# Kernel tuning notes

Measured on AMD Instinct MI355X. Metric: run time of the kernel, lower is better.

Reference implementation:

```python
import jax, jax.numpy as jnp
import numpy as np

N = 100000
N1 = 12500  # N // K clusters after one downsample
K = 8
CHANNELS = [256, 128, 64, 32, 3]


def _conv(f, idx, kern, bias, act):
    # gather K neighbors and flatten: [M, K*Cin]
    g = f[idx].reshape(idx.shape[0], -1)
    out = g @ kern.T + bias
    return jax.nn.sigmoid(out) if act else out


def setup_inputs() -> dict:
    key = jax.random.key(0)
    ks = jax.random.split(key, 16)
    inp = {
        "features": jax.random.normal(ks[0], (N, 256), dtype=jnp.float32),
        "knn_idx0": jax.random.randint(ks[1], (N, K), 0, N, dtype=jnp.int32),
        "knn_idx1": jax.random.randint(ks[2], (N1, K), 0, N1, dtype=jnp.int32),
        "labels": jax.random.randint(ks[3], (N,), 0, N1, dtype=jnp.int32),
    }
    cin = 256
    for i, cout in enumerate(CHANNELS):
        inp[f"k{i}"] = jax.random.normal(ks[4 + i], (cout, K * cin), dtype=jnp.float32) * 0.1
        inp[f"b{i}"] = jnp.zeros((1, cout), dtype=jnp.float32)
        cin = cout
    return inp


def reference(features, knn_idx0, knn_idx1, labels, k0, b0, k1, b1, k2, b2, k3, b3, k4, b4):
    f = features
    # layer 0 (full resolution)
    f = _conv(f, knn_idx0, k0, b0, act=True)
    # layer 1: downsample via scatter-mean over kmeans labels
    s = jax.ops.segment_sum(f, labels, num_segments=N1)
    cnt = jax.ops.segment_sum(jnp.ones((f.shape[0], 1), f.dtype), labels, num_segments=N1)
    f = s / jnp.maximum(cnt, 1.0)
    f = _conv(f, knn_idx1, k1, b1, act=True)
    # layer 2 (coarse resolution)
    f = _conv(f, knn_idx1, k2, b2, act=True)
    # layer 3: upsample by indexing cluster features back to points
    f = f[labels]
    f = _conv(f, knn_idx0, k3, b3, act=True)
    # layer 4: final, no sigmoid
    f = _conv(f, knn_idx0, k4, b4, act=False)
    return f
```

## Files before the change

kernel.cpp:

```cpp
#include <hip/hip_runtime.h>
#include <hip/hip_bf16.h>


typedef __attribute__((ext_vector_type(8))) _Float16 f16x8;
typedef __attribute__((ext_vector_type(4))) float f32x4;
typedef __attribute__((ext_vector_type(8))) unsigned short u16x8;

#define NPTS 100000
#define N1PTS 12500

__device__ __forceinline__ void gload_lds16(const unsigned short* g, unsigned short* l) {
  __builtin_amdgcn_global_load_lds(
      (const __attribute__((address_space(1))) void*)g,
      (__attribute__((address_space(3))) void*)l, 16, 0, 0);
}

__device__ __forceinline__ int swz(int r, int k) {
  return r * 64 + ((((k >> 3) ^ r) & 7) << 3) + (k & 7);
}

__device__ __forceinline__ unsigned short f16bits(float x) {
  return __builtin_bit_cast(unsigned short, (_Float16)x);
}

__global__ void prepack_w(const float* __restrict__ W, unsigned short* __restrict__ out,
                          int n) {
  int i = blockIdx.x * 256 + threadIdx.x;
  if (i < n) out[i] = f16bits(W[i]);
}

__global__ void prepack_w0(const float* __restrict__ W, unsigned short* __restrict__ out) {
  const int tid = blockIdx.x * 256 + threadIdx.x;
  const int l = tid & 63;
  const int s = (tid >> 6) & 1;
  const int n = (tid >> 7) & 3;
  const int w = (tid >> 9) & 3;
  const int c = tid >> 11;
  const int co = w * 64 + n * 16 + (l & 15);
  const int k = c * 64 + s * 32 + ((l >> 4) << 3);
  const float* src = W + (size_t)co * 2048 + k;
  u16x8 h;
#pragma unroll
  for (int e = 0; e < 8; ++e) h[e] = f16bits(src[e]);
  ((u16x8*)out)[tid] = h;
}

__global__ void prepack_feat(const float* __restrict__ F, unsigned short* __restrict__ out,
                             int n8) {
  int i = blockIdx.x * 256 + threadIdx.x;
  if (i >= n8) return;
  const float4* s = (const float4*)(F + (size_t)i * 8);
  float4 v0 = s[0], v1 = s[1];
  float x[8] = {v0.x, v0.y, v0.z, v0.w, v1.x, v1.y, v1.z, v1.w};
  u16x8 o;
#pragma unroll
  for (int e = 0; e < 8; ++e) o[e] = f16bits(x[e]);
  ((u16x8*)out)[i] = o;
}

__global__ void count_labels(const int* __restrict__ labels, int* __restrict__ cnt) {
  int i = blockIdx.x * 256 + threadIdx.x;
  if (i < NPTS) atomicAdd(&cnt[labels[i]], 1);
}

__global__ void compose_idx(const int* __restrict__ knn0, const int* __restrict__ labels,
                            int* __restrict__ out) {
  int i = blockIdx.x * 256 + threadIdx.x;
  if (i < NPTS * 8) out[i] = labels[knn0[i]];
}

__global__ void finalize_pool(const int* __restrict__ pool, const int* __restrict__ cnt,
                              unsigned short* __restrict__ out) {
  int i = blockIdx.x * 256 + threadIdx.x;
  if (i >= N1PTS * 256) return;
  float denom = fmaxf((float)cnt[i >> 8], 1.0f);
  out[i] = f16bits(((float)pool[i]) * (1.0f / 16777216.0f) / denom);
}

__global__ void finalize_splitk(const int* __restrict__ acc, const float* __restrict__ bias,
                                unsigned short* __restrict__ out, int n, int cmask) {
  int i = blockIdx.x * 256 + threadIdx.x;
  if (i >= n) return;
  float z = ((float)acc[i]) * (1.0f / 4194304.0f) + bias[i & cmask];
  out[i] = f16bits(1.0f / (1.0f + expf(-z)));
}

__global__ __launch_bounds__(256, 3) void conv0_gemm(
    const unsigned short* __restrict__ F16, const int* __restrict__ idx,
    const int* __restrict__ lab, const unsigned short* __restrict__ Wpk,
    const float* __restrict__ bias, int* __restrict__ pool) {
  __shared__ alignas(16) unsigned short sA[4][64 * 64];

  const int t = threadIdx.x;
  const int w = t >> 6, l = t & 63;
  const int lr = l & 15, lh = l >> 4;
  const int row0 = blockIdx.x * 64;

  const int srow8 = l >> 3;
  const int sseg_src = (l & 7) ^ (srow8 & 7);

  const unsigned ldsbase = (unsigned)(uintptr_t)&sA[0][0];
  unsigned aoff[4][2];
#pragma unroll
  for (int m = 0; m < 4; ++m)
#pragma unroll
    for (int s = 0; s < 2; ++s)
      aoff[m][s] =
          ldsbase + (((m * 16 + lr) * 64 + ((((s << 2) + lh) ^ (lr & 7)) << 3)) << 1);

  const f16x8* wp8 = (const f16x8*)Wpk + (size_t)w * 512 + l;

  auto ldnb = [&](int cc, int q) -> int {
    int grow = row0 + w * 16 + q * 8 + srow8;
    grow = grow < NPTS ? grow : NPTS - 1;
    return idx[grow * 8 + ((cc & 31) >> 2)];
  };
  auto stage_q = [&](int cc, int nb, int q) {
    const unsigned short* gp =
        F16 + ((size_t)nb << 8) + ((cc & 3) << 6) + sseg_src * 8;
    unsigned short* lp = &sA[cc & 3][(w * 16 + q * 8) * 64];
    gload_lds16(gp, lp);
  };

  f32x4 acc[4][4] = {};
  f16x8 bh[2][4];

  int n00 = ldnb(0, 0), n01 = ldnb(0, 1);
  int n10 = ldnb(1, 0), n11 = ldnb(1, 1);
  int nc0 = ldnb(2, 0), nc1 = ldnb(2, 1);
  __builtin_amdgcn_sched_barrier(0);
#pragma unroll
  for (int s = 0; s < 2; ++s)
#pragma unroll
    for (int n = 0; n < 4; ++n) bh[s][n] = wp8[n * 128 + s * 64];
  __builtin_amdgcn_sched_barrier(0);
  stage_q(0, n00, 0); stage_q(0, n01, 1);
  __builtin_amdgcn_sched_barrier(0);
  stage_q(1, n10, 0); stage_q(1, n11, 1);
  __builtin_amdgcn_sched_barrier(0);
  asm volatile("s_waitcnt vmcnt(2)" ::: "memory");
  __builtin_amdgcn_sched_barrier(0);
  __builtin_amdgcn_s_barrier();
  __builtin_amdgcn_sched_barrier(0);

#pragma unroll 1
  for (int c = 0; c < 32; ++c) {
    const unsigned bb = (unsigned)((c & 3) << 13);

    f16x8 av[4][2];
    asm volatile("ds_read_b128 %0, %1" : "=v"(av[0][0]) : "v"(aoff[0][0] + bb));
    asm volatile("ds_read_b128 %0, %1" : "=v"(av[1][0]) : "v"(aoff[1][0] + bb));
    asm volatile("ds_read_b128 %0, %1" : "=v"(av[2][0]) : "v"(aoff[2][0] + bb));
    asm volatile("ds_read_b128 %0, %1" : "=v"(av[3][0]) : "v"(aoff[3][0] + bb));
    asm volatile("ds_read_b128 %0, %1" : "=v"(av[0][1]) : "v"(aoff[0][1] + bb));
    asm volatile("ds_read_b128 %0, %1" : "=v"(av[1][1]) : "v"(aoff[1][1] + bb));
    asm volatile("ds_read_b128 %0, %1" : "=v"(av[2][1]) : "v"(aoff[2][1] + bb));
    asm volatile("ds_read_b128 %0, %1" : "=v"(av[3][1]) : "v"(aoff[3][1] + bb));
    __builtin_amdgcn_sched_barrier(0);
    asm volatile("s_waitcnt lgkmcnt(4)");
    __builtin_amdgcn_sched_barrier(0);

    const f16x8* wpn = wp8 + 2048;
    f16x8 bnext[2][4];
#pragma unroll
    for (int s = 0; s < 2; ++s)
#pragma unroll
      for (int n = 0; n < 4; ++n) bnext[s][n] = wpn[n * 128 + s * 64];
#pragma unroll
    for (int n = 0; n < 4; ++n)
#pragma unroll
      for (int m = 0; m < 4; ++m)
        acc[m][n] =
            __builtin_amdgcn_mfma_f32_16x16x32_f16(av[m][0], bh[0][n], acc[m][n], 0, 0, 0);
    __builtin_amdgcn_sched_barrier(0);
    asm volatile("s_waitcnt lgkmcnt(0)");
    __builtin_amdgcn_sched_barrier(0);
#pragma unroll
    for (int n = 0; n < 4; ++n)
#pragma unroll
      for (int m = 0; m < 4; ++m)
        acc[m][n] =
            __builtin_amdgcn_mfma_f32_16x16x32_f16(av[m][1], bh[1][n], acc[m][n], 0, 0, 0);
#pragma unroll
    for (int s = 0; s < 2; ++s)
#pragma unroll
      for (int n = 0; n < 4; ++n) bh[s][n] = bnext[s][n];
    __builtin_amdgcn_sched_barrier(0);

    const int cn = (c + 3) & 31;
    int t0 = ldnb(cn, 0), t1 = ldnb(cn, 1);
    __builtin_amdgcn_sched_barrier(0);
    const int cg = (c + 2) & 31;
    stage_q(cg, nc0, 0); stage_q(cg, nc1, 1);
    __builtin_amdgcn_sched_barrier(0);
    asm volatile("s_waitcnt vmcnt(12)" ::: "memory");
    __builtin_amdgcn_sched_barrier(0);
    __builtin_amdgcn_s_barrier();
    __builtin_amdgcn_sched_barrier(0);
    nc0 = t0; nc1 = t1;
    wp8 = wpn;
  }
  asm volatile("s_waitcnt vmcnt(0)" ::: "memory");

  float bv[4];
#pragma unroll
  for (int n = 0; n < 4; ++n) bv[n] = bias[w * 64 + n * 16 + lr];
#pragma unroll
  for (int m = 0; m < 4; ++m) {
#pragma unroll
    for (int r = 0; r < 4; ++r) {
      const int i = row0 + m * 16 + lh * 4 + r;
      if (i < NPTS) {
        const int lb = lab[i];
#pragma unroll
        for (int n = 0; n < 4; ++n) {
          float z = acc[m][n][r] + bv[n];
          z = 1.0f / (1.0f + expf(-z));
          atomicAdd(&pool[(size_t)lb * 256 + (w * 64 + n * 16 + lr)],
                    __float2int_rn(z * 16777216.0f));
        }
      }
    }
  }
}

template <bool ACT, bool OUT16, bool SPLITK>
__global__ __launch_bounds__(256, 2) void conv_gemm(
    const unsigned short* __restrict__ act16, const int* __restrict__ idx,
    const unsigned short* __restrict__ Wf, const float* __restrict__ bias,
    void* __restrict__ outp, int M, int cinShift, int Cout, int Ktot, int ksl) {
  __shared__ alignas(16) unsigned short sAh[4096];
  __shared__ alignas(16) unsigned short sBh[4096];

  const int Cin = 1 << cinShift;
  const int t = threadIdx.x;
  const int bm = blockIdx.x, bn = blockIdx.y;
  const int kbase = SPLITK ? blockIdx.z * ksl : 0;

  const int sr = t >> 2;
  const int kseg = (t & 3) << 4;
  const int ai = bm * 64 + sr;
  const int bco = bn * 64 + sr;

  f32x4 acc[4] = {};

  const int nch = ksl >> 6;
  for (int kc = 0; kc < nch; ++kc) {
    const int kg = kbase + (kc << 6) + kseg;

    u16x8 h0 = {}, h1 = {};
    if (ai < M) {
      const int j = kg >> cinShift;
      const int nbv = idx[ai * 8 + j];
      const unsigned short* src = act16 + ((size_t)nbv << cinShift) + (kg & (Cin - 1));
      h0 = ((const u16x8*)src)[0];
      h1 = ((const u16x8*)src)[1];
    }

    u16x8 bh0 = {}, bh1 = {};
    if (bco < Cout) {
      const unsigned short* sw = Wf + (size_t)bco * Ktot + kg;
      bh0 = ((const u16x8*)sw)[0];
      bh1 = ((const u16x8*)sw)[1];
    }

    __syncthreads();
    const int w0 = swz(sr, kseg), w1 = swz(sr, kseg + 8);
    *(u16x8*)&sAh[w0] = h0; *(u16x8*)&sAh[w1] = h1;
    *(u16x8*)&sBh[w0] = bh0; *(u16x8*)&sBh[w1] = bh1;
    __syncthreads();

    const int l = t & 63;
    const int lr = l & 15, lh = l >> 4;
    const int wid = t >> 6;
#pragma unroll
    for (int s = 0; s < 2; ++s) {
      const int kb = s * 32 + lh * 8;
      const int boff = swz(wid * 16 + lr, kb);
      f16x8 bh = *(const f16x8*)&sBh[boff];
#pragma unroll
      for (int m = 0; m < 4; ++m) {
        const int aoff = swz(m * 16 + lr, kb);
        f16x8 ah = *(const f16x8*)&sAh[aoff];
        acc[m] = __builtin_amdgcn_mfma_f32_16x16x32_f16(ah, bh, acc[m], 0, 0, 0);
      }
    }
  }

  const int l = t & 63, wid = t >> 6;
  const int lr = l & 15, lh = l >> 4;
  const int co = bn * 64 + wid * 16 + lr;
  if (co < Cout) {
    const float bvv = SPLITK ? 0.0f : bias[co];
#pragma unroll
    for (int m = 0; m < 4; ++m) {
#pragma unroll
      for (int r = 0; r < 4; ++r) {
        const int i = bm * 64 + m * 16 + lh * 4 + r;
        if (i < M) {
          float z = acc[m][r] + bvv;
          if (SPLITK) {
            atomicAdd(&((int*)outp)[(size_t)i * Cout + co],
                      __float2int_rn(z * 4194304.0f));
          } else {
            if (ACT) z = 1.0f / (1.0f + expf(-z));
            if (OUT16)
              ((unsigned short*)outp)[(size_t)i * Cout + co] = f16bits(z);
            else
              ((float*)outp)[(size_t)i * Cout + co] = z;
          }
        }
      }
    }
  }
}

extern "C" void kernel_launch(void* const* d_in, const int* in_sizes, int n_in,
                              void* d_out, int out_size, void* d_ws, size_t ws_size,
                              hipStream_t stream) {
  const float* features = (const float*)d_in[0];
  const int* knn0 = (const int*)d_in[1];
  const int* knn1 = (const int*)d_in[2];
  const int* labels = (const int*)d_in[3];
  const float* kw[5] = {(const float*)d_in[4], (const float*)d_in[6],
                        (const float*)d_in[8], (const float*)d_in[10],
                        (const float*)d_in[12]};
  const float* bw[5] = {(const float*)d_in[5], (const float*)d_in[7],
                        (const float*)d_in[9], (const float*)d_in[11],
                        (const float*)d_in[13]};

  char* ws = (char*)d_ws;
  size_t off = 0;
  auto alloc = [&](size_t bytes) -> void* {
    void* p = ws + off;
    off = (off + bytes + 255) & ~(size_t)255;
    return p;
  };
  unsigned short* Wpk0 = (unsigned short*)alloc((size_t)(524288 + 16384) * 2);
  const int wsz14[4] = {262144, 65536, 16384, 768};
  const int woff14[4] = {0, 262144, 327680, 344064};
  unsigned short* W14 = (unsigned short*)alloc((size_t)344832 * 2);
  int* pool = (int*)alloc((size_t)N1PTS * 256 * 4);
  int* cnt = (int*)alloc((size_t)N1PTS * 4);
  int* f1i = (int*)alloc((size_t)N1PTS * 128 * 4);
  int* f2i = (int*)alloc((size_t)N1PTS * 64 * 4);
  unsigned short* pooled = (unsigned short*)alloc((size_t)N1PTS * 256 * 2);
  unsigned short* f1 = (unsigned short*)alloc((size_t)N1PTS * 128 * 2);
  unsigned short* f2 = (unsigned short*)alloc((size_t)N1PTS * 64 * 2);
  int* idx3 = (int*)alloc((size_t)NPTS * 8 * 4);
  unsigned short* F16 = (unsigned short*)alloc((size_t)NPTS * 256 * 2);
  unsigned short* f3 = (unsigned short*)pool;
  if (off > ws_size) return;

  prepack_w0<<<256, 256, 0, stream>>>(kw[0], Wpk0);
  for (int i = 0; i < 4; ++i)
    prepack_w<<<(wsz14[i] + 255) / 256, 256, 0, stream>>>(kw[i + 1], W14 + woff14[i], wsz14[i]);
  prepack_feat<<<(NPTS * 256 / 8 + 255) / 256, 256, 0, stream>>>(features, F16, NPTS * 256 / 8);
  compose_idx<<<(NPTS * 8 + 255) / 256, 256, 0, stream>>>(knn0, labels, idx3);

  hipMemsetAsync(pool, 0, (size_t)((char*)pooled - (char*)pool), stream);
  count_labels<<<(NPTS + 255) / 256, 256, 0, stream>>>(labels, cnt);

  conv0_gemm<<<1563, 256, 0, stream>>>(F16, knn0, labels, Wpk0, bw[0], pool);

  finalize_pool<<<(N1PTS * 256 + 255) / 256, 256, 0, stream>>>(pool, cnt, pooled);

  dim3 blk(256);
  conv_gemm<true, true, true><<<dim3(196, 2, 4), blk, 0, stream>>>(
      pooled, knn1, W14 + woff14[0], bw[1], f1i, N1PTS, 8, 128, 2048, 512);
  finalize_splitk<<<(N1PTS * 128 + 255) / 256, 256, 0, stream>>>(
      f1i, bw[1], f1, N1PTS * 128, 127);
  conv_gemm<true, true, true><<<dim3(196, 1, 4), blk, 0, stream>>>(
      f1, knn1, W14 + woff14[1], bw[2], f2i, N1PTS, 7, 64, 1024, 256);
  finalize_splitk<<<(N1PTS * 64 + 255) / 256, 256, 0, stream>>>(
      f2i, bw[2], f2, N1PTS * 64, 63);
  conv_gemm<true, true, false><<<dim3(1563, 1), blk, 0, stream>>>(
      f2, idx3, W14 + woff14[2], bw[3], f3, NPTS, 6, 32, 512, 512);
  conv_gemm<false, false, false><<<dim3(1563, 1), blk, 0, stream>>>(
      f3, knn0, W14 + woff14[3], bw[4], (float*)d_out, NPTS, 5, 3, 256, 256);
}
```

Before: 298.7 us.

## Deepen conv0 gather pipeline, prefetch LDS reads, and merge prep kernels

The conv0 GEMM main loop now stages three chunks ahead instead of two. It issues the next chunk's LDS reads right after the MFMAs, so they overlap the following barrier and global loads, and it loads neighbour indices through precomputed row pointers. The four weight prepack launches become one kernel, and the compose_idx and count_labels kernels are fused, which cuts launch count. The cost is a tighter vmcnt wait and more LDS buffer slots in flight, plus a higher risk of ordering or race bugs in the hand-scheduled pipeline.

Result: faster. 286.8 us (-4.0%).

```diff
diff --git a/kernel.cpp b/kernel.cpp
--- a/kernel.cpp
+++ b/kernel.cpp
@@ -21,12 +21,6 @@
 
 __device__ __forceinline__ unsigned short f16bits(float x) {
   return __builtin_bit_cast(unsigned short, (_Float16)x);
-}
-
-__global__ void prepack_w(const float* __restrict__ W, unsigned short* __restrict__ out,
-                          int n) {
-  int i = blockIdx.x * 256 + threadIdx.x;
-  if (i < n) out[i] = f16bits(W[i]);
 }
 
 __global__ void prepack_w0(const float* __restrict__ W, unsigned short* __restrict__ out) {
@@ -45,6 +39,19 @@
   ((u16x8*)out)[tid] = h;
 }
 
+__global__ void prepack_w14(const float* __restrict__ k1, const float* __restrict__ k2,
+                            const float* __restrict__ k3, const float* __restrict__ k4,
+                            unsigned short* __restrict__ out) {
+  int i = blockIdx.x * 256 + threadIdx.x;
+  if (i >= 344832) return;
+  float v;
+  if (i < 262144) v = k1[i];
+  else if (i < 327680) v = k2[i - 262144];
+  else if (i < 344064) v = k3[i - 327680];
+  else v = k4[i - 344064];
+  out[i] = f16bits(v);
+}
+
 __global__ void prepack_feat(const float* __restrict__ F, unsigned short* __restrict__ out,
                              int n8) {
   int i = blockIdx.x * 256 + threadIdx.x;
@@ -58,15 +65,11 @@
   ((u16x8*)out)[i] = o;
 }
 
-__global__ void count_labels(const int* __restrict__ labels, int* __restrict__ cnt) {
-  int i = blockIdx.x * 256 + threadIdx.x;
+__global__ void fused_aux(const int* __restrict__ knn0, const int* __restrict__ labels,
+                          int* __restrict__ idx3, int* __restrict__ cnt) {
+  int i = blockIdx.x * 256 + threadIdx.x;
+  if (i < NPTS * 8) idx3[i] = labels[knn0[i]];
   if (i < NPTS) atomicAdd(&cnt[labels[i]], 1);
-}
-
-__global__ void compose_idx(const int* __restrict__ knn0, const int* __restrict__ labels,
-                            int* __restrict__ out) {
-  int i = blockIdx.x * 256 + threadIdx.x;
-  if (i < NPTS * 8) out[i] = labels[knn0[i]];
 }
 
 __global__ void finalize_pool(const int* __restrict__ pool, const int* __restrict__ cnt,
@@ -108,13 +111,13 @@
       aoff[m][s] =
           ldsbase + (((m * 16 + lr) * 64 + ((((s << 2) + lh) ^ (lr & 7)) << 3)) << 1);
 
+  int g0 = row0 + w * 16 + srow8;      g0 = g0 < NPTS ? g0 : NPTS - 1;
+  int g1 = row0 + w * 16 + 8 + srow8;  g1 = g1 < NPTS ? g1 : NPTS - 1;
+  const int* idxp0 = idx + g0 * 8;
+  const int* idxp1 = idx + g1 * 8;
+
   const f16x8* wp8 = (const f16x8*)Wpk + (size_t)w * 512 + l;
 
-  auto ldnb = [&](int cc, int q) -> int {
-    int grow = row0 + w * 16 + q * 8 + srow8;
-    grow = grow < NPTS ? grow : NPTS - 1;
-    return idx[grow * 8 + ((cc & 31) >> 2)];
-  };
   auto stage_q = [&](int cc, int nb, int q) {
     const unsigned short* gp =
         F16 + ((size_t)nb << 8) + ((cc & 3) << 6) + sseg_src * 8;
@@ -124,40 +127,37 @@
 
   f32x4 acc[4][4] = {};
   f16x8 bh[2][4];
-
-  int n00 = ldnb(0, 0), n01 = ldnb(0, 1);
-  int n10 = ldnb(1, 0), n11 = ldnb(1, 1);
-  int nc0 = ldnb(2, 0), nc1 = ldnb(2, 1);
+  f16x8 av[4][2];
+
+  int n0 = idxp0[0], n1 = idxp1[0];
   __builtin_amdgcn_sched_barrier(0);
 #pragma unroll
   for (int s = 0; s < 2; ++s)
 #pragma unroll
     for (int n = 0; n < 4; ++n) bh[s][n] = wp8[n * 128 + s * 64];
   __builtin_amdgcn_sched_barrier(0);
-  stage_q(0, n00, 0); stage_q(0, n01, 1);
-  __builtin_amdgcn_sched_barrier(0);
-  stage_q(1, n10, 0); stage_q(1, n11, 1);
-  __builtin_amdgcn_sched_barrier(0);
+  stage_q(0, n0, 0); stage_q(0, n1, 1);
+  stage_q(1, n0, 0); stage_q(1, n1, 1);
+  stage_q(2, n0, 0); stage_q(2, n1, 1);
+  __builtin_amdgcn_sched_barrier(0);
+  int nc0 = n0, nc1 = n1;
   asm volatile("s_waitcnt vmcnt(2)" ::: "memory");
   __builtin_amdgcn_sched_barrier(0);
   __builtin_amdgcn_s_barrier();
+  __builtin_amdgcn_sched_barrier(0);
+  asm volatile("ds_read_b128 %0, %1" : "=v"(av[0][0]) : "v"(aoff[0][0]));
+  asm volatile("ds_read_b128 %0, %1" : "=v"(av[1][0]) : "v"(aoff[1][0]));
+  asm volatile("ds_read_b128 %0, %1" : "=v"(av[2][0]) : "v"(aoff[2][0]));
+  asm volatile("ds_read_b128 %0, %1" : "=v"(av[3][0]) : "v"(aoff[3][0]));
+  asm volatile("ds_read_b128 %0, %1" : "=v"(av[0][1]) : "v"(aoff[0][1]));
+  asm volatile("ds_read_b128 %0, %1" : "=v"(av[1][1]) : "v"(aoff[1][1]));
+  asm volatile("ds_read_b128 %0, %1" : "=v"(av[2][1]) : "v"(aoff[2][1]));
+  asm volatile("ds_read_b128 %0, %1" : "=v"(av[3][1]) : "v"(aoff[3][1]));
   __builtin_amdgcn_sched_barrier(0);
 
 #pragma unroll 1
   for (int c = 0; c < 32; ++c) {
-    const unsigned bb = (unsigned)((c & 3) << 13);
-
-    f16x8 av[4][2];
-    asm volatile("ds_read_b128 %0, %1" : "=v"(av[0][0]) : "v"(aoff[0][0] + bb));
-    asm volatile("ds_read_b128 %0, %1" : "=v"(av[1][0]) : "v"(aoff[1][0] + bb));
-    asm volatile("ds_read_b128 %0, %1" : "=v"(av[2][0]) : "v"(aoff[2][0] + bb));
-    asm volatile("ds_read_b128 %0, %1" : "=v"(av[3][0]) : "v"(aoff[3][0] + bb));
-    asm volatile("ds_read_b128 %0, %1" : "=v"(av[0][1]) : "v"(aoff[0][1] + bb));
-    asm volatile("ds_read_b128 %0, %1" : "=v"(av[1][1]) : "v"(aoff[1][1] + bb));
-    asm volatile("ds_read_b128 %0, %1" : "=v"(av[2][1]) : "v"(aoff[2][1] + bb));
-    asm volatile("ds_read_b128 %0, %1" : "=v"(av[3][1]) : "v"(aoff[3][1] + bb));
-    __builtin_amdgcn_sched_barrier(0);
-    asm volatile("s_waitcnt lgkmcnt(4)");
+    asm volatile("s_waitcnt lgkmcnt(0)");
     __builtin_amdgcn_sched_barrier(0);
 
     const f16x8* wpn = wp8 + 2048;
@@ -172,35 +172,44 @@
       for (int m = 0; m < 4; ++m)
         acc[m][n] =
             __builtin_amdgcn_mfma_f32_16x16x32_f16(av[m][0], bh[0][n], acc[m][n], 0, 0, 0);
-    __builtin_amdgcn_sched_barrier(0);
-    asm volatile("s_waitcnt lgkmcnt(0)");
-    __builtin_amdgcn_sched_barrier(0);
 #pragma unroll
     for (int n = 0; n < 4; ++n)
 #pragma unroll
       for (int m = 0; m < 4; ++m)
         acc[m][n] =
             __builtin_amdgcn_mfma_f32_16x16x32_f16(av[m][1], bh[1][n], acc[m][n], 0, 0, 0);
+    __builtin_amdgcn_sched_barrier(0);
+
+    const unsigned bb2 = (unsigned)(((c + 1) & 3) << 13);
+    asm volatile("ds_read_b128 %0, %1" : "=v"(av[0][0]) : "v"(aoff[0][0] + bb2));
+    asm volatile("ds_read_b128 %0, %1" : "=v"(av[1][0]) : "v"(aoff[1][0] + bb2));
+    asm volatile("ds_read_b128 %0, %1" : "=v"(av[2][0]) : "v"(aoff[2][0] + bb2));
+    asm volatile("ds_read_b128 %0, %1" : "=v"(av[3][0]) : "v"(aoff[3][0] + bb2));
+    asm volatile("ds_read_b128 %0, %1" : "=v"(av[0][1]) : "v"(aoff[0][1] + bb2));
+    asm volatile("ds_read_b128 %0, %1" : "=v"(av[1][1]) : "v"(aoff[1][1] + bb2));
+    asm volatile("ds_read_b128 %0, %1" : "=v"(av[2][1]) : "v"(aoff[2][1] + bb2));
+    asm volatile("ds_read_b128 %0, %1" : "=v"(av[3][1]) : "v"(aoff[3][1] + bb2));
+    __builtin_amdgcn_sched_barrier(0);
+
+    const int jn = ((c + 4) & 31) >> 2;
+    int t0 = idxp0[jn], t1 = idxp1[jn];
+    __builtin_amdgcn_sched_barrier(0);
+    const int cg = (c + 3) & 31;
+    stage_q(cg, nc0, 0); stage_q(cg, nc1, 1);
+    __builtin_amdgcn_sched_barrier(0);
 #pragma unroll
     for (int s = 0; s < 2; ++s)
 #pragma unroll
       for (int n = 0; n < 4; ++n) bh[s][n] = bnext[s][n];
     __builtin_amdgcn_sched_barrier(0);
-
-    const int cn = (c + 3) & 31;
-    int t0 = ldnb(cn, 0), t1 = ldnb(cn, 1);
-    __builtin_amdgcn_sched_barrier(0);
-    const int cg = (c + 2) & 31;
-    stage_q(cg, nc0, 0); stage_q(cg, nc1, 1);
-    __builtin_amdgcn_sched_barrier(0);
-    asm volatile("s_waitcnt vmcnt(12)" ::: "memory");
+    asm volatile("s_waitcnt vmcnt(4)" ::: "memory");
     __builtin_amdgcn_sched_barrier(0);
     __builtin_amdgcn_s_barrier();
     __builtin_amdgcn_sched_barrier(0);
     nc0 = t0; nc1 = t1;
     wp8 = wpn;
   }
-  asm volatile("s_waitcnt vmcnt(0)" ::: "memory");
+  asm volatile("s_waitcnt vmcnt(0) lgkmcnt(0)" ::: "memory");
 
   float bv[4];
 #pragma unroll
@@ -337,7 +346,6 @@
     return p;
   };
   unsigned short* Wpk0 = (unsigned short*)alloc((size_t)(524288 + 16384) * 2);
-  const int wsz14[4] = {262144, 65536, 16384, 768};
   const int woff14[4] = {0, 262144, 327680, 344064};
   unsigned short* W14 = (unsigned short*)alloc((size_t)344832 * 2);
   int* pool = (int*)alloc((size_t)N1PTS * 256 * 4);
@@ -353,13 +361,11 @@
   if (off > ws_size) return;
 
   prepack_w0<<<256, 256, 0, stream>>>(kw[0], Wpk0);
-  for (int i = 0; i < 4; ++i)
-    prepack_w<<<(wsz14[i] + 255) / 256, 256, 0, stream>>>(kw[i + 1], W14 + woff14[i], wsz14[i]);
+  prepack_w14<<<1347, 256, 0, stream>>>(kw[1], kw[2], kw[3], kw[4], W14);
   prepack_feat<<<(NPTS * 256 / 8 + 255) / 256, 256, 0, stream>>>(features, F16, NPTS * 256 / 8);
-  compose_idx<<<(NPTS * 8 + 255) / 256, 256, 0, stream>>>(knn0, labels, idx3);
 
   hipMemsetAsync(pool, 0, (size_t)((char*)pooled - (char*)pool), stream);
-  count_labels<<<(NPTS + 255) / 256, 256, 0, stream>>>(labels, cnt);
+  fused_aux<<<(NPTS * 8 + 255) / 256, 256, 0, stream>>>(knn0, labels, idx3, cnt);
 
   conv0_gemm<<<1563, 256, 0, stream>>>(F16, knn0, labels, Wpk0, bw[0], pool);
 
```
